# Kernel optimization log

Measured on AMD Instinct MI355X. Metric: run time of the kernel, lower is better.

The kernel has to match this reference:

```python
import jax, jax.numpy as jnp
import numpy as np

B, S, D, H = 2, 2048, 2048, 16
HD = D // H
THETA = 10000.0


def _rope(t, pos):
    # t: [B, H, S, hd], pos: [S] int -> rotary position embedding (half-split form)
    half = t.shape[-1] // 2
    inv_freq = 1.0 / (THETA ** (jnp.arange(half, dtype=jnp.float32) / half))
    ang = pos[:, None].astype(jnp.float32) * inv_freq[None, :]  # [S, half]
    cos, sin = jnp.cos(ang), jnp.sin(ang)
    t1, t2 = t[..., :half], t[..., half:]
    return jnp.concatenate([t1 * cos - t2 * sin, t1 * sin + t2 * cos], axis=-1)


def setup_inputs() -> dict:
    key = jax.random.key(0)
    ks = jax.random.split(key, 5)
    scale = 1.0 / np.sqrt(D)
    return {
        "x": jax.random.normal(ks[0], (B, S, D), dtype=jnp.float32),
        "Wq": jax.random.normal(ks[1], (D, D), dtype=jnp.float32) * scale,
        "Wk": jax.random.normal(ks[2], (D, D), dtype=jnp.float32) * scale,
        "Wv": jax.random.normal(ks[3], (D, D), dtype=jnp.float32) * scale,
        "Wo": jax.random.normal(ks[4], (D, D), dtype=jnp.float32) * scale,
        "token_positions": jnp.arange(S, dtype=jnp.int32),
    }


def reference(x, Wq, Wk, Wv, Wo, token_positions):
    b, s, d = x.shape
    # fused QKV projection (nn.Linear: y = x @ W.T)
    q = (x @ Wq.T).reshape(b, s, H, HD).transpose(0, 2, 1, 3)  # [B,H,S,hd]
    k = (x @ Wk.T).reshape(b, s, H, HD).transpose(0, 2, 1, 3)
    v = (x @ Wv.T).reshape(b, s, H, HD).transpose(0, 2, 1, 3)
    q = _rope(q, token_positions)
    k = _rope(k, token_positions)
    scale = 1.0 / np.sqrt(HD)
    scores = jnp.einsum("bhqd,bhkd->bhqk", q, k) * scale  # [B,H,S,S]
    causal = jnp.triu(jnp.ones((s, s), dtype=bool), k=1)
    scores = jnp.where(causal, jnp.float32(-jnp.inf), scores)
    attn = jax.nn.softmax(scores, axis=-1)
    o = jnp.einsum("bhqk,bhkd->bhqd", attn, v)  # [B,H,S,hd]
    o = o.transpose(0, 2, 1, 3).reshape(b, s, d)
    return o @ Wo.T
```

## Files before the change

### kernel.cpp

```cpp
#include <hip/hip_runtime.h>
#include <math.h>

#define B_  2
#define S_  2048
#define D_  2048
#define H_  16
#define HD_ 128

using u16 = unsigned short;
using u32 = unsigned int;
typedef __attribute__((ext_vector_type(4))) float f32x4;
typedef __attribute__((ext_vector_type(8))) short bf16x8;
using u16x4_t = __attribute__((ext_vector_type(4))) unsigned short;
using u16x8_t = __attribute__((ext_vector_type(8))) unsigned short;
typedef __attribute__((ext_vector_type(2))) u32 u32x2;
typedef __attribute__((ext_vector_type(4))) u32 u32x4;

__device__ __forceinline__ u16 f2bf(float f) {
  u32 u = __builtin_bit_cast(u32, f);
  u32 r = u + 0x7fffu + ((u >> 16) & 1u);
  return (u16)(r >> 16);
}
__device__ __forceinline__ float bf2f(u16 x) {
  u32 u = ((u32)x) << 16;
  return __builtin_bit_cast(float, u);
}
__device__ __forceinline__ void async_copy16(const u16* g, u16* l) {
  __builtin_amdgcn_global_load_lds((const __attribute__((address_space(1))) u32*)g,
                                   (__attribute__((address_space(3))) u32*)l, 16, 0, 0);
}

__global__ void cvt_all(const float* __restrict__ x, const float* __restrict__ Wq,
                        const float* __restrict__ Wk, const float* __restrict__ Wv,
                        const float* __restrict__ Wo, u16* __restrict__ dst) {
  const int i = (blockIdx.x * blockDim.x + threadIdx.x) * 4;
  if (i >= 25165824) return;
  const float* src;
  int off;
  if (i < (1 << 23)) { src = x; off = i; }
  else {
    const int wi = i - (1 << 23);
    const int which = wi >> 22;
    off = wi & ((1 << 22) - 1);
    src = (which == 0) ? Wq : (which == 1) ? Wk : (which == 2) ? Wv : Wo;
  }
  float4 v = *(const float4*)(src + off);
  u16x4_t o;
  o[0] = f2bf(v.x); o[1] = f2bf(v.y); o[2] = f2bf(v.z); o[3] = f2bf(v.w);
  *(u16x4_t*)(dst + i) = o;
}

__global__ void rope_table(const int* __restrict__ pos, float2* __restrict__ tab) {
  int t = blockIdx.x * blockDim.x + threadIdx.x;
  if (t >= S_ * 64) return;
  int s = t >> 6, i = t & 63;
  float freq = expf(-(float)i * (9.210340371976184f / 64.0f));
  float ang = (float)pos[s] * freq;
  tab[t] = make_float2(cosf(ang), sinf(ang));
}

__global__ void rope_k(u16* __restrict__ K, const float2* __restrict__ tab) {
  int t = blockIdx.x * blockDim.x + threadIdx.x;
  int g = t & 15;
  int bsh = t >> 4;
  int h = bsh & (H_ - 1);
  int bs = bsh >> 4;
  int s = bs & (S_ - 1);
  size_t base = (size_t)bs * D_ + (size_t)h * HD_;
  int d2 = g * 4;
  const float2* tb = &tab[s * 64 + d2];
  float2 cs[4];
  #pragma unroll
  for (int j = 0; j < 4; ++j) cs[j] = tb[j];
  u16x4_t a = *(u16x4_t*)(K + base + d2);
  u16x4_t c = *(u16x4_t*)(K + base + 64 + d2);
  u16x4_t ra, rc;
  #pragma unroll
  for (int j = 0; j < 4; ++j) {
    float t1 = bf2f(a[j]), t2 = bf2f(c[j]);
    ra[j] = f2bf(t1 * cs[j].x - t2 * cs[j].y);
    rc[j] = f2bf(t1 * cs[j].y + t2 * cs[j].x);
  }
  *(u16x4_t*)(K + base + d2) = ra;
  *(u16x4_t*)(K + base + 64 + d2) = rc;
}

template <bool F32OUT>
__global__ __launch_bounds__(256, 2)
void gemm_bt(const u16* __restrict__ A, const u16* __restrict__ Bt,
             void* __restrict__ Cout, int M, int N, int K) {
  __shared__ u16 lA[3][128 * 32];
  __shared__ u16 lB[3][128 * 32];
  const int tid = threadIdx.x;
  const int lane = tid & 63;
  const int w = tid >> 6;
  const int wr = w >> 1, wc = w & 1;
  const int bm = blockIdx.x * 128;
  const int bn = blockIdx.y * 128;
  const int fr = lane & 15, fq = lane >> 4;
  const int KT = K >> 5;
  f32x4 acc[4][4] = {};

  auto stage = [&](int buf, int kt) {
    const int k0 = kt << 5;
    #pragma unroll
    for (int c = w; c < 8; c += 4) {
      const int r = c * 16 + (lane >> 2);
      const int col = ((lane & 3) ^ ((r >> 1) & 3)) * 8;
      async_copy16(A + (size_t)(bm + r) * K + k0 + col, &lA[buf][c * 512]);
      async_copy16(Bt + (size_t)(bn + r) * K + k0 + col, &lB[buf][c * 512]);
    }
  };

  stage(0, 0);
  stage(1, 1);
  asm volatile("s_waitcnt vmcnt(4)" ::: "memory");
  __builtin_amdgcn_s_barrier();
  asm volatile("" ::: "memory");

  int p = 0, sb = 2;
  #pragma unroll 1
  for (int kt = 0; kt < KT; ++kt) {
    if (kt + 2 < KT) stage(sb, kt + 2);
    bf16x8 af[4], bfr[4];
    #pragma unroll
    for (int i = 0; i < 4; ++i) {
      const int ra = wr * 64 + i * 16 + fr;
      const int rb = wc * 64 + i * 16 + fr;
      af[i]  = *(const bf16x8*)&lA[p][ra * 32 + ((fq ^ ((ra >> 1) & 3)) * 8)];
      bfr[i] = *(const bf16x8*)&lB[p][rb * 32 + ((fq ^ ((rb >> 1) & 3)) * 8)];
    }
    #pragma unroll
    for (int i = 0; i < 4; ++i)
      #pragma unroll
      for (int j = 0; j < 4; ++j)
        acc[i][j] = __builtin_amdgcn_mfma_f32_16x16x32_bf16(af[i], bfr[j], acc[i][j], 0, 0, 0);
    if (kt + 1 < KT) {
      if (kt + 2 < KT) asm volatile("s_waitcnt vmcnt(4)" ::: "memory");
      else             asm volatile("s_waitcnt vmcnt(0)" ::: "memory");
      __builtin_amdgcn_s_barrier();
      asm volatile("" ::: "memory");
    }
    p  = (p == 2) ? 0 : p + 1;
    sb = (sb == 2) ? 0 : sb + 1;
  }
  #pragma unroll
  for (int i = 0; i < 4; ++i)
    #pragma unroll
    for (int j = 0; j < 4; ++j) {
      const int row = bm + wr * 64 + i * 16 + fq * 4;
      const int col = bn + wc * 64 + j * 16 + fr;
      #pragma unroll
      for (int r = 0; r < 4; ++r) {
        const float v = acc[i][j][r];
        if (F32OUT) ((float*)Cout)[(size_t)(row + r) * N + col] = v;
        else        ((u16*)Cout)[(size_t)(row + r) * N + col] = f2bf(v);
      }
    }
}

__global__ __launch_bounds__(256, 2)
void gemm_qkv3(const u16* __restrict__ A, const u16* __restrict__ Bt,
               u16* __restrict__ Qo, u16* __restrict__ Ko, u16* __restrict__ Vo) {
  __shared__ u16 lA[3][128 * 32];
  __shared__ u16 lB[3][128 * 32];
  const int tid = threadIdx.x;
  const int lane = tid & 63;
  const int w = tid >> 6;
  const int wr = w >> 1, wc = w & 1;
  const int bm = blockIdx.x * 128;
  const int bn = blockIdx.y * 128;
  const int fr = lane & 15, fq = lane >> 4;
  const int K = D_;
  const int KT = K >> 5;
  f32x4 acc[4][4] = {};

  auto stage = [&](int buf, int kt) {
    const int k0 = kt << 5;
    #pragma unroll
    for (int c = w; c < 8; c += 4) {
      const int r = c * 16 + (lane >> 2);
      const int col = ((lane & 3) ^ ((r >> 1) & 3)) * 8;
      async_copy16(A + (size_t)(bm + r) * K + k0 + col, &lA[buf][c * 512]);
      async_copy16(Bt + (size_t)(bn + r) * K + k0 + col, &lB[buf][c * 512]);
    }
  };

  stage(0, 0);
  stage(1, 1);
  asm volatile("s_waitcnt vmcnt(4)" ::: "memory");
  __builtin_amdgcn_s_barrier();
  asm volatile("" ::: "memory");

  int p = 0, sb = 2;
  #pragma unroll 1
  for (int kt = 0; kt < KT; ++kt) {
    if (kt + 2 < KT) stage(sb, kt + 2);
    bf16x8 af[4], bfr[4];
    #pragma unroll
    for (int i = 0; i < 4; ++i) {
      const int ra = wr * 64 + i * 16 + fr;
      const int rb = wc * 64 + i * 16 + fr;
      af[i]  = *(const bf16x8*)&lA[p][ra * 32 + ((fq ^ ((ra >> 1) & 3)) * 8)];
      bfr[i] = *(const bf16x8*)&lB[p][rb * 32 + ((fq ^ ((rb >> 1) & 3)) * 8)];
    }
    #pragma unroll
    for (int i = 0; i < 4; ++i)
      #pragma unroll
      for (int j = 0; j < 4; ++j)
        acc[i][j] = __builtin_amdgcn_mfma_f32_16x16x32_bf16(af[i], bfr[j], acc[i][j], 0, 0, 0);
    if (kt + 1 < KT) {
      if (kt + 2 < KT) asm volatile("s_waitcnt vmcnt(4)" ::: "memory");
      else             asm volatile("s_waitcnt vmcnt(0)" ::: "memory");
      __builtin_amdgcn_s_barrier();
      asm volatile("" ::: "memory");
    }
    p  = (p == 2) ? 0 : p + 1;
    sb = (sb == 2) ? 0 : sb + 1;
  }
  u16* out = (bn < 2048) ? Qo : (bn < 4096) ? Ko : Vo;
  const int bnl = bn & 2047;
  #pragma unroll
  for (int i = 0; i < 4; ++i)
    #pragma unroll
    for (int j = 0; j < 4; ++j) {
      const int row = bm + wr * 64 + i * 16 + fq * 4;
      const int col = bnl + wc * 64 + j * 16 + fr;
      #pragma unroll
      for (int r = 0; r < 4; ++r)
        out[(size_t)(row + r) * D_ + col] = f2bf(acc[i][j][r]);
    }
}

#define QB 64
#define KB 32
#define PLD 36

__global__ __launch_bounds__(256, 2)
void attn_fwd(const u16* __restrict__ Qg, const u16* __restrict__ Kg,
              const u16* __restrict__ Vg, const float2* __restrict__ tab,
              u16* __restrict__ po0, u16* __restrict__ po1, float2* __restrict__ ml) {
  __shared__ u16 lK[2][KB * HD_];
  __shared__ u16 lV[2][HD_ * 40];
  __shared__ u16 lP[4][16 * PLD];
  const int tid = threadIdx.x;
  const int lane = tid & 63;
  const int w = tid >> 6;
  const int fr = lane & 15, fq = lane >> 4;
  const int xA = blockIdx.x;
  const int bh = blockIdx.y;
  const int split = blockIdx.z;
  const size_t base = (size_t)(bh >> 4) * S_ * D_ + (size_t)(bh & 15) * HD_;
  const int qA = xA * QB, qB = (31 - xA) * QB;
  const int ntA = (qA + QB) / KB;
  const int ntB = (qB + QB) / KB;
  const int c = (ntA <= 16) ? (33 - ntA) : 16;
  const int t0 = split ? c : 0;
  const int t1 = split ? ntB : c;
  const float kscale = 0.08838834764831843f * 1.4426950408889634f;

  bf16x8 qfA[4], qfB[4];
  {
    const u16* qpa = Qg + base + (size_t)(qA + w * 16 + fr) * D_ + fq * 8;
    const u16* qpb = Qg + base + (size_t)(qB + w * 16 + fr) * D_ + fq * 8;
    #pragma unroll
    for (int kk = 0; kk < 4; ++kk) {
      qfA[kk] = *(const bf16x8*)(qpa + kk * 32);
      qfB[kk] = *(const bf16x8*)(qpb + kk * 32);
    }
    const float2* tA = &tab[(qA + w * 16 + fr) * 64 + fq * 8];
    const float2* tB = &tab[(qB + w * 16 + fr) * 64 + fq * 8];
    #pragma unroll
    for (int kk = 0; kk < 2; ++kk)
      #pragma unroll
      for (int j = 0; j < 8; ++j) {
        const float2 ca = tA[kk * 32 + j];
        float t1 = bf2f((u16)qfA[kk][j]), t2 = bf2f((u16)qfA[kk + 2][j]);
        qfA[kk][j]     = (short)f2bf(t1 * ca.x - t2 * ca.y);
        qfA[kk + 2][j] = (short)f2bf(t1 * ca.y + t2 * ca.x);
        const float2 cb = tB[kk * 32 + j];
        t1 = bf2f((u16)qfB[kk][j]); t2 = bf2f((u16)qfB[kk + 2][j]);
        qfB[kk][j]     = (short)f2bf(t1 * cb.x - t2 * cb.y);
        qfB[kk + 2][j] = (short)f2bf(t1 * cb.y + t2 * cb.x);
      }
  }
  f32x4 oA[8] = {}, oB[8] = {};
  float mAs = -INFINITY, lAs = 0.f, mBs = -INFINITY, lBs = 0.f;

  auto stageK = [&](int buf, int kv0) {
    #pragma unroll
    for (int cc = w; cc < 8; cc += 4) {
      const int row = cc * 4 + (lane >> 4);
      const int slot = (lane & 15) ^ (row & 7);
      async_copy16(Kg + base + (size_t)(kv0 + row) * D_ + slot * 8, &lK[buf][cc * 512]);
    }
  };
  const int srow = tid >> 3, sc0 = (tid & 7) * 16;
  const u32 swz = (u32)((sc0 >> 4) & 7) << 4;
  const u32 rb = (u32)srow * 2;
  u16x8_t rv0, rv1;
  auto loadV = [&](int kv0) {
    const u16* gv = Vg + base + (size_t)(kv0 + srow) * D_ + sc0;
    rv0 = *(const u16x8_t*)gv; rv1 = *(const u16x8_t*)(gv + 8);
  };
  auto writeV = [&](int buf) {
    char* lv = (char*)&lV[buf][0];
    #pragma unroll
    for (int j = 0; j < 8; ++j) {
      *(u16*)(lv + ((((u32)(sc0 + j) * 80) + rb) ^ swz))     = rv0[j];
      *(u16*)(lv + ((((u32)(sc0 + 8 + j) * 80) + rb) ^ swz)) = rv1[j];
    }
  };

  auto softmax_sw = [&](const f32x4& s0, const f32x4& s1, float& mrow, float& lrow,
                        f32x4* o, int q0t, int kv0) {
    const int qg = q0t + w * 16 + fr;
    const bool notfull = (kv0 + KB - 1 > q0t);
    float v[8];
    #pragma unroll
    for (int r = 0; r < 4; ++r) {
      v[r]     = s0[r] * kscale;
      v[4 + r] = s1[r] * kscale;
      if (notfull) {
        if (kv0 + fq * 4 + r > qg)      v[r]     = -INFINITY;
        if (kv0 + 16 + fq * 4 + r > qg) v[4 + r] = -INFINITY;
      }
    }
    float mx = fmaxf(fmaxf(fmaxf(v[0], v[1]), fmaxf(v[2], v[3])),
                     fmaxf(fmaxf(v[4], v[5]), fmaxf(v[6], v[7])));
    mx = fmaxf(mx, __shfl_xor(mx, 16));
    mx = fmaxf(mx, __shfl_xor(mx, 32));
    const int nogrow = (mx <= mrow + 12.f);
    if (!__all(nogrow)) {
      const float mn = fmaxf(mrow, mx);
      const float al = exp2f(mrow - mn);
      mrow = mn;
      lrow *= al;
      #pragma unroll
      for (int r = 0; r < 4; ++r) {
        const float ab = __shfl(al, fq * 4 + r);
        #pragma unroll
        for (int nb = 0; nb < 8; ++nb) o[nb][r] *= ab;
      }
    }
    float p[8];
    #pragma unroll
    for (int j = 0; j < 8; ++j) p[j] = exp2f(v[j] - mrow);
    float rs = ((p[0] + p[1]) + (p[2] + p[3])) + ((p[4] + p[5]) + (p[6] + p[7]));
    rs += __shfl_xor(rs, 16);
    rs += __shfl_xor(rs, 32);
    lrow += rs;
    #pragma unroll
    for (int r = 0; r < 4; ++r) {
      lP[w][fr * PLD + fq * 4 + r]      = f2bf(p[r]);
      lP[w][fr * PLD + 16 + fq * 4 + r] = f2bf(p[4 + r]);
    }
  };

  auto pv = [&](f32x4* o, const bf16x8* vf) {
    u32x2 pa0 = *(const u32x2*)&lP[w][fr * PLD + fq * 8];
    u32x2 pa1 = *(const u32x2*)&lP[w][fr * PLD + fq * 8 + 4];
    u32x4 pc; pc[0] = pa0[0]; pc[1] = pa0[1]; pc[2] = pa1[0]; pc[3] = pa1[1];
    const bf16x8 pa = __builtin_bit_cast(bf16x8, pc);
    #pragma unroll
    for (int nb = 0; nb < 8; ++nb)
      o[nb] = __builtin_amdgcn_mfma_f32_16x16x32_bf16(pa, vf[nb], o[nb], 0, 0, 0);
  };

  stageK(0, t0 * KB);
  loadV(t0 * KB);
  writeV(0);

  for (int t = t0; t < t1; ++t) {
    const int kv0 = t * KB;
    const int cur = (t - t0) & 1, nxt = cur ^ 1;
    __syncthreads();
    if (t + 1 < t1) {
      stageK(nxt, kv0 + KB);
      loadV(kv0 + KB);
    }

    const bool doA = (t < ntA);
    f32x4 sA0 = {}, sA1 = {}, sB0 = {}, sB1 = {};
    #pragma unroll
    for (int kk = 0; kk < 4; ++kk) {
      const int sl = ((kk * 4 + fq) ^ (fr & 7)) * 16;
      bf16x8 k0f = *(const bf16x8*)((const char*)&lK[cur][0] + fr * 256 + sl);
      bf16x8 k1f = *(const bf16x8*)((const char*)&lK[cur][0] + (16 + fr) * 256 + sl);
      if (doA) {
        sA0 = __builtin_amdgcn_mfma_f32_16x16x32_bf16(k0f, qfA[kk], sA0, 0, 0, 0);
        sA1 = __builtin_amdgcn_mfma_f32_16x16x32_bf16(k1f, qfA[kk], sA1, 0, 0, 0);
      }
      sB0 = __builtin_amdgcn_mfma_f32_16x16x32_bf16(k0f, qfB[kk], sB0, 0, 0, 0);
      sB1 = __builtin_amdgcn_mfma_f32_16x16x32_bf16(k1f, qfB[kk], sB1, 0, 0, 0);
    }

    bf16x8 vf[8];
    #pragma unroll
    for (int nb = 0; nb < 8; ++nb) {
      const u32 off = (((u32)(nb * 16 + fr) * 80) + (u32)fq * 16) ^ ((u32)nb << 4);
      vf[nb] = *(const bf16x8*)((const char*)&lV[cur][0] + off);
    }

    if (doA) { softmax_sw(sA0, sA1, mAs, lAs, oA, qA, kv0); pv(oA, vf); }
    softmax_sw(sB0, sB1, mBs, lBs, oB, qB, kv0);
    pv(oB, vf);

    if (t + 1 < t1) writeV(nxt);
  }

  u16* po = split ? po1 : po0;
  float2* mlp = ml + (size_t)split * (B_ * H_ * S_) + (size_t)bh * S_;
  if (lane < 16) {
    mlp[qA + w * 16 + fr] = make_float2(mAs, lAs);
    mlp[qB + w * 16 + fr] = make_float2(mBs, lBs);
  }
  #pragma unroll
  for (int r = 0; r < 4; ++r) {
    const int rowA = qA + w * 16 + fq * 4 + r;
    const int rowB = qB + w * 16 + fq * 4 + r;
    u16* orA = po + base + (size_t)rowA * D_;
    u16* orB = po + base + (size_t)rowB * D_;
    #pragma unroll
    for (int nb = 0; nb < 8; ++nb) {
      orA[nb * 16 + fr] = f2bf(oA[nb][r]);
      orB[nb * 16 + fr] = f2bf(oB[nb][r]);
    }
  }
}

__global__ void attn_combine(const u16* __restrict__ po0, const u16* __restrict__ po1,
                             const float2* __restrict__ ml, u16* __restrict__ Og) {
  const int idx = blockIdx.x * blockDim.x + threadIdx.x;
  const int d8 = (idx & 15) * 8;
  const int row = idx >> 4;
  const int bh = row >> 11, s = row & (S_ - 1);
  const float2 v0 = ml[row];
  const float2 v1 = ml[B_ * H_ * S_ + row];
  const float m = fmaxf(v0.x, v1.x);
  const float e0 = exp2f(v0.x - m), e1 = exp2f(v1.x - m);
  const float inv = 1.0f / (v0.y * e0 + v1.y * e1);
  const size_t off = (size_t)(bh >> 4) * S_ * D_ + (size_t)s * D_ + (bh & 15) * HD_ + d8;
  u16x8_t a = *(const u16x8_t*)(po0 + off);
  u16x8_t b = *(const u16x8_t*)(po1 + off);
  u16x8_t o;
  #pragma unroll
  for (int j = 0; j < 8; ++j)
    o[j] = f2bf((bf2f(a[j]) * e0 + bf2f(b[j]) * e1) * inv);
  *(u16x8_t*)(Og + off) = o;
}

extern "C" void kernel_launch(void* const* d_in, const int* in_sizes, int n_in,
                              void* d_out, int out_size, void* d_ws, size_t ws_size,
                              hipStream_t stream) {
  const float* x  = (const float*)d_in[0];
  const float* Wq = (const float*)d_in[1];
  const float* Wk = (const float*)d_in[2];
  const float* Wv = (const float*)d_in[3];
  const float* Wo = (const float*)d_in[4];
  const int* pos  = (const int*)d_in[5];

  char* p = (char*)d_ws;
  u16* xb  = (u16*)p; p += (size_t)B_ * S_ * D_ * 2;
  u16* Wqb = (u16*)p; p += (size_t)D_ * D_ * 2;
  u16* Wkb = (u16*)p; p += (size_t)D_ * D_ * 2;
  u16* Wvb = (u16*)p; p += (size_t)D_ * D_ * 2;
  u16* Wob = (u16*)p; p += (size_t)D_ * D_ * 2;
  u16* Qb  = (u16*)p; p += (size_t)B_ * S_ * D_ * 2;
  u16* Kb  = (u16*)p; p += (size_t)B_ * S_ * D_ * 2;
  u16* Vb  = (u16*)p; p += (size_t)B_ * S_ * D_ * 2;
  float2* tab = (float2*)p; p += (size_t)S_ * 64 * sizeof(float2);
  float2* ml  = (float2*)p; p += (size_t)2 * B_ * H_ * S_ * sizeof(float2);
  u16* po0 = xb;
  u16* po1 = Wqb;
  u16* Ob  = Qb;

  cvt_all<<<24576, 256, 0, stream>>>(x, Wq, Wk, Wv, Wo, xb);
  rope_table<<<(S_ * 64) / 256, 256, 0, stream>>>(pos, tab);

  gemm_qkv3<<<dim3(B_ * S_ / 128, 48), 256, 0, stream>>>(xb, Wqb, Qb, Kb, Vb);

  rope_k<<<(B_ * S_ * H_ * 16) / 256, 256, 0, stream>>>(Kb, tab);

  attn_fwd<<<dim3(16, B_ * H_, 2), 256, 0, stream>>>(Qb, Kb, Vb, tab, po0, po1, ml);
  attn_combine<<<(B_ * H_ * S_ * 16) / 256, 256, 0, stream>>>(po0, po1, ml, Ob);

  gemm_bt<true><<<dim3(B_ * S_ / 128, D_ / 128), 256, 0, stream>>>(Ob, Wob, (float*)d_out, B_ * S_, D_, D_);
}
```

Measured before the change: 314.0 us.

## Drop split-KV attention and combine kernel, normalize in-kernel, fold scale into Q

Removes the two-way KV split in attention and the separate combine kernel. Each block now processes its full causal KV range and normalizes its output by 1/l before writing bf16 directly. It also folds the softmax scale into the rotated Q fragments and packs the P writes to LDS into 64-bit stores. This saves the partial-output and m/l traffic plus one launch, but halves the grid to 512 blocks, which gives less latency hiding and no load balancing across splits. Prescaling Q before bf16 rounding changes numerics slightly.

Result: faster. 295.8 us (-5.8%).

```diff
diff --git a/kernel.cpp b/kernel.cpp
--- a/kernel.cpp
+++ b/kernel.cpp
@@ -239,7 +239,7 @@
 __global__ __launch_bounds__(256, 2)
 void attn_fwd(const u16* __restrict__ Qg, const u16* __restrict__ Kg,
               const u16* __restrict__ Vg, const float2* __restrict__ tab,
-              u16* __restrict__ po0, u16* __restrict__ po1, float2* __restrict__ ml) {
+              u16* __restrict__ Og) {
   __shared__ u16 lK[2][KB * HD_];
   __shared__ u16 lV[2][HD_ * 40];
   __shared__ u16 lP[4][16 * PLD];
@@ -249,14 +249,10 @@
   const int fr = lane & 15, fq = lane >> 4;
   const int xA = blockIdx.x;
   const int bh = blockIdx.y;
-  const int split = blockIdx.z;
   const size_t base = (size_t)(bh >> 4) * S_ * D_ + (size_t)(bh & 15) * HD_;
   const int qA = xA * QB, qB = (31 - xA) * QB;
   const int ntA = (qA + QB) / KB;
   const int ntB = (qB + QB) / KB;
-  const int c = (ntA <= 16) ? (33 - ntA) : 16;
-  const int t0 = split ? c : 0;
-  const int t1 = split ? ntB : c;
   const float kscale = 0.08838834764831843f * 1.4426950408889634f;
 
   bf16x8 qfA[4], qfB[4];
@@ -276,12 +272,12 @@
       for (int j = 0; j < 8; ++j) {
         const float2 ca = tA[kk * 32 + j];
         float t1 = bf2f((u16)qfA[kk][j]), t2 = bf2f((u16)qfA[kk + 2][j]);
-        qfA[kk][j]     = (short)f2bf(t1 * ca.x - t2 * ca.y);
-        qfA[kk + 2][j] = (short)f2bf(t1 * ca.y + t2 * ca.x);
+        qfA[kk][j]     = (short)f2bf((t1 * ca.x - t2 * ca.y) * kscale);
+        qfA[kk + 2][j] = (short)f2bf((t1 * ca.y + t2 * ca.x) * kscale);
         const float2 cb = tB[kk * 32 + j];
         t1 = bf2f((u16)qfB[kk][j]); t2 = bf2f((u16)qfB[kk + 2][j]);
-        qfB[kk][j]     = (short)f2bf(t1 * cb.x - t2 * cb.y);
-        qfB[kk + 2][j] = (short)f2bf(t1 * cb.y + t2 * cb.x);
+        qfB[kk][j]     = (short)f2bf((t1 * cb.x - t2 * cb.y) * kscale);
+        qfB[kk + 2][j] = (short)f2bf((t1 * cb.y + t2 * cb.x) * kscale);
       }
   }
   f32x4 oA[8] = {}, oB[8] = {};
@@ -319,8 +315,8 @@
     float v[8];
     #pragma unroll
     for (int r = 0; r < 4; ++r) {
-      v[r]     = s0[r] * kscale;
-      v[4 + r] = s1[r] * kscale;
+      v[r]     = s0[r];
+      v[4 + r] = s1[r];
       if (notfull) {
         if (kv0 + fq * 4 + r > qg)      v[r]     = -INFINITY;
         if (kv0 + 16 + fq * 4 + r > qg) v[4 + r] = -INFINITY;
@@ -350,11 +346,13 @@
     rs += __shfl_xor(rs, 16);
     rs += __shfl_xor(rs, 32);
     lrow += rs;
-    #pragma unroll
-    for (int r = 0; r < 4; ++r) {
-      lP[w][fr * PLD + fq * 4 + r]      = f2bf(p[r]);
-      lP[w][fr * PLD + 16 + fq * 4 + r] = f2bf(p[4 + r]);
-    }
+    u32x2 pk0, pk1;
+    pk0[0] = (u32)f2bf(p[0]) | ((u32)f2bf(p[1]) << 16);
+    pk0[1] = (u32)f2bf(p[2]) | ((u32)f2bf(p[3]) << 16);
+    pk1[0] = (u32)f2bf(p[4]) | ((u32)f2bf(p[5]) << 16);
+    pk1[1] = (u32)f2bf(p[6]) | ((u32)f2bf(p[7]) << 16);
+    *(u32x2*)&lP[w][fr * PLD + fq * 4]      = pk0;
+    *(u32x2*)&lP[w][fr * PLD + 16 + fq * 4] = pk1;
   };
 
   auto pv = [&](f32x4* o, const bf16x8* vf) {
@@ -367,15 +365,15 @@
       o[nb] = __builtin_amdgcn_mfma_f32_16x16x32_bf16(pa, vf[nb], o[nb], 0, 0, 0);
   };
 
-  stageK(0, t0 * KB);
-  loadV(t0 * KB);
+  stageK(0, 0);
+  loadV(0);
   writeV(0);
 
-  for (int t = t0; t < t1; ++t) {
+  for (int t = 0; t < ntB; ++t) {
     const int kv0 = t * KB;
-    const int cur = (t - t0) & 1, nxt = cur ^ 1;
+    const int cur = t & 1, nxt = cur ^ 1;
     __syncthreads();
-    if (t + 1 < t1) {
+    if (t + 1 < ntB) {
       stageK(nxt, kv0 + KB);
       loadV(kv0 + KB);
     }
@@ -406,48 +404,25 @@
     softmax_sw(sB0, sB1, mBs, lBs, oB, qB, kv0);
     pv(oB, vf);
 
-    if (t + 1 < t1) writeV(nxt);
-  }
-
-  u16* po = split ? po1 : po0;
-  float2* mlp = ml + (size_t)split * (B_ * H_ * S_) + (size_t)bh * S_;
-  if (lane < 16) {
-    mlp[qA + w * 16 + fr] = make_float2(mAs, lAs);
-    mlp[qB + w * 16 + fr] = make_float2(mBs, lBs);
-  }
+    if (t + 1 < ntB) writeV(nxt);
+  }
+
+  const float invA = 1.0f / lAs;
+  const float invB = 1.0f / lBs;
   #pragma unroll
   for (int r = 0; r < 4; ++r) {
+    const float ia = __shfl(invA, fq * 4 + r);
+    const float ib = __shfl(invB, fq * 4 + r);
     const int rowA = qA + w * 16 + fq * 4 + r;
     const int rowB = qB + w * 16 + fq * 4 + r;
-    u16* orA = po + base + (size_t)rowA * D_;
-    u16* orB = po + base + (size_t)rowB * D_;
+    u16* orA = Og + base + (size_t)rowA * D_;
+    u16* orB = Og + base + (size_t)rowB * D_;
     #pragma unroll
     for (int nb = 0; nb < 8; ++nb) {
-      orA[nb * 16 + fr] = f2bf(oA[nb][r]);
-      orB[nb * 16 + fr] = f2bf(oB[nb][r]);
-    }
-  }
-}
-
-__global__ void attn_combine(const u16* __restrict__ po0, const u16* __restrict__ po1,
-                             const float2* __restrict__ ml, u16* __restrict__ Og) {
-  const int idx = blockIdx.x * blockDim.x + threadIdx.x;
-  const int d8 = (idx & 15) * 8;
-  const int row = idx >> 4;
-  const int bh = row >> 11, s = row & (S_ - 1);
-  const float2 v0 = ml[row];
-  const float2 v1 = ml[B_ * H_ * S_ + row];
-  const float m = fmaxf(v0.x, v1.x);
-  const float e0 = exp2f(v0.x - m), e1 = exp2f(v1.x - m);
-  const float inv = 1.0f / (v0.y * e0 + v1.y * e1);
-  const size_t off = (size_t)(bh >> 4) * S_ * D_ + (size_t)s * D_ + (bh & 15) * HD_ + d8;
-  u16x8_t a = *(const u16x8_t*)(po0 + off);
-  u16x8_t b = *(const u16x8_t*)(po1 + off);
-  u16x8_t o;
-  #pragma unroll
-  for (int j = 0; j < 8; ++j)
-    o[j] = f2bf((bf2f(a[j]) * e0 + bf2f(b[j]) * e1) * inv);
-  *(u16x8_t*)(Og + off) = o;
+      orA[nb * 16 + fr] = f2bf(oA[nb][r] * ia);
+      orB[nb * 16 + fr] = f2bf(oB[nb][r] * ib);
+    }
+  }
 }
 
 extern "C" void kernel_launch(void* const* d_in, const int* in_sizes, int n_in,
@@ -470,10 +445,7 @@
   u16* Kb  = (u16*)p; p += (size_t)B_ * S_ * D_ * 2;
   u16* Vb  = (u16*)p; p += (size_t)B_ * S_ * D_ * 2;
   float2* tab = (float2*)p; p += (size_t)S_ * 64 * sizeof(float2);
-  float2* ml  = (float2*)p; p += (size_t)2 * B_ * H_ * S_ * sizeof(float2);
-  u16* po0 = xb;
-  u16* po1 = Wqb;
-  u16* Ob  = Qb;
+  u16* Ob = Qb;
 
   cvt_all<<<24576, 256, 0, stream>>>(x, Wq, Wk, Wv, Wo, xb);
   rope_table<<<(S_ * 64) / 256, 256, 0, stream>>>(pos, tab);
@@ -482,8 +454,7 @@
 
   rope_k<<<(B_ * S_ * H_ * 16) / 256, 256, 0, stream>>>(Kb, tab);
 
-  attn_fwd<<<dim3(16, B_ * H_, 2), 256, 0, stream>>>(Qb, Kb, Vb, tab, po0, po1, ml);
-  attn_combine<<<(B_ * H_ * S_ * 16) / 256, 256, 0, stream>>>(po0, po1, ml, Ob);
+  attn_fwd<<<dim3(16, B_ * H_), 256, 0, stream>>>(Qb, Kb, Vb, tab, Ob);
 
   gemm_bt<true><<<dim3(B_ * S_ / 128, D_ / 128), 256, 0, stream>>>(Ob, Wob, (float*)d_out, B_ * S_, D_, D_);
 }
```
